# Kernel optimization log

Measured on AMD Instinct MI355X. Metric: run time of the kernel, lower is better.

## Reference

```python
import jax, jax.numpy as jnp
import numpy as np
from jax import lax

DIM = 256
HEADS = 8
C3 = DIM * 3 // 4  # 192
C1 = DIM // 4      # 64


def conv1x1(x, w):
    # x: [b,c,h,w], w: [o,c] (1x1 conv, no bias)
    return jnp.einsum('bchw,oc->bohw', x, w)


def dwconv3x3(x, w):
    # x: [b,c,h,w], w: [c,1,3,3] depthwise
    return lax.conv_general_dilated(
        x, w, window_strides=(1, 1), padding='SAME',
        feature_group_count=x.shape[1],
        dimension_numbers=('NCHW', 'OIHW', 'NCHW'))


def l2norm(x, eps=1e-12):
    # torch F.normalize: x / max(||x||, eps) along last dim
    n = jnp.sqrt(jnp.sum(x * x, axis=-1, keepdims=True))
    return x / jnp.maximum(n, eps)


def setup_inputs() -> dict:
    key = jax.random.key(0)
    ks = jax.random.split(key, 10)
    s = 0.02
    return {
        'x': jax.random.normal(ks[0], (4, DIM, 128, 128), jnp.float32),
        'k_v': jax.random.normal(ks[1], (4, 256), jnp.float32),
        'temperature': jnp.ones((HEADS, 1, 1), jnp.float32),
        'w_kR': jax.random.normal(ks[2], (C3, 192), jnp.float32) * s,
        'w_kI': jax.random.normal(ks[3], (C1, 64), jnp.float32) * s,
        'w_qR': jax.random.normal(ks[4], (DIM, C3), jnp.float32) * s,
        'w_qdw': jax.random.normal(ks[5], (DIM, 1, 3, 3), jnp.float32) * s,
        'w_kvI': jax.random.normal(ks[6], (2 * DIM, C1), jnp.float32) * s,
        'w_kvdw': jax.random.normal(ks[7], (2 * DIM, 1, 3, 3), jnp.float32) * s,
        'w_proj': jax.random.normal(ks[8], (DIM, DIM), jnp.float32) * s,
    }


def reference(x, k_v, temperature, w_kR, w_kI, w_qR, w_qdw, w_kvI, w_kvdw, w_proj):
    b, c, h, w = x.shape
    # FiLM-style modulation: x * kv + x
    kvr = (k_v[:, :192] @ w_kR.T)[:, :, None, None]  # [b, C3, 1, 1]
    kvi = (k_v[:, 192:] @ w_kI.T)[:, :, None, None]  # [b, C1, 1, 1]
    x_r = x[:, :C3] * kvr + x[:, :C3]
    x_i = x[:, C3:] * kvi + x[:, C3:]
    # QKV projections
    q = dwconv3x3(conv1x1(x_r, w_qR), w_qdw)          # [b, dim, h, w]
    kv = dwconv3x3(conv1x1(x_i, w_kvI), w_kvdw)       # [b, 2*dim, h, w]
    k, v = jnp.split(kv, 2, axis=1)
    hd = DIM // HEADS
    hw = h * w
    q = q.reshape(b, HEADS, hd, hw)
    k = k.reshape(b, HEADS, hd, hw)
    v = v.reshape(b, HEADS, hd, hw)
    # channel-wise (transposed) attention with L2 norm + temperature
    q = l2norm(q)
    k = l2norm(k)
    attn = jnp.einsum('bhcn,bhdn->bhcd', q, k) * temperature  # [b,H,hd,hd]
    attn = jax.nn.softmax(attn, axis=-1)
    out = jnp.einsum('bhcd,bhdn->bhcn', attn, v)
    out = out.reshape(b, DIM, h, w)
    return conv1x1(out, w_proj)
```

## Files before the change

### kernel.cpp

```cpp
#include <hip/hip_runtime.h>
#include <math.h>

#define HW 16384

typedef unsigned int uint;
typedef short bfrag __attribute__((ext_vector_type(8)));
typedef float f32x4 __attribute__((ext_vector_type(4)));

union FragCvt { uint4 u; bfrag v; };

__device__ inline uint pack2bf(float a, float b) {
  uint ua = __builtin_bit_cast(uint, a);
  uint ub = __builtin_bit_cast(uint, b);
  ua = (ua + 0x7FFFu + ((ua >> 16) & 1u)) >> 16;
  ub = (ub + 0x7FFFu + ((ub >> 16) & 1u)) & 0xFFFF0000u;
  return ua | ub;
}

__device__ inline void cvt_hilo(float4 a, float4 b, bfrag& hi, bfrag& lo) {
  float v0[8] = {a.x, a.y, a.z, a.w, b.x, b.y, b.z, b.w};
  uint hv[4], lv[4];
  #pragma unroll
  for (int i = 0; i < 4; ++i) {
    float x0 = v0[2 * i], x1 = v0[2 * i + 1];
    uint h = pack2bf(x0, x1);
    float h0 = __builtin_bit_cast(float, h << 16);
    float h1 = __builtin_bit_cast(float, h & 0xFFFF0000u);
    hv[i] = h;
    lv[i] = pack2bf(x0 - h0, x1 - h1);
  }
  FragCvt ch, cl;
  ch.u = make_uint4(hv[0], hv[1], hv[2], hv[3]);
  cl.u = make_uint4(lv[0], lv[1], lv[2], lv[3]);
  hi = ch.v;
  lo = cl.v;
}

#define LDS_BARRIER() do { \
  asm volatile("s_waitcnt lgkmcnt(0)" ::: "memory"); \
  __builtin_amdgcn_s_barrier(); \
} while (0)

__global__ __launch_bounds__(256) void mod_kernel(
    const float* __restrict__ kv, const float* __restrict__ wkR,
    const float* __restrict__ wkI, float* __restrict__ mod,
    float* __restrict__ S)
{
  int b = blockIdx.x;
  int c = threadIdx.x;
  float4 z4 = make_float4(0.f, 0.f, 0.f, 0.f);
  float4* sp = (float4*)(S + (((size_t)b * 256 + c) << 5));
  #pragma unroll
  for (int i = 0; i < 8; ++i) sp[i] = z4;

  const float* kvb = kv + b * 256;
  float s = 0.f;
  if (c < 192) {
    const float* wr = wkR + c * 192;
    for (int j = 0; j < 192; ++j) s += kvb[j] * wr[j];
  } else {
    const float* wi = wkI + (c - 192) * 64;
    for (int j = 0; j < 64; ++j) s += kvb[192 + j] * wi[j];
  }
  mod[b * 256 + c] = 1.f + s;
}

__device__ __forceinline__ void mgemm_body(
    const float* __restrict__ Wt, int ldW,
    const float* __restrict__ Xt,
    const float* __restrict__ modc,
    float* __restrict__ Yt,
    int K, int t, unsigned short* Al, unsigned short* Bl, float* Ml)
{
  int w = t >> 6, l = t & 63;
  int wm = (w >> 1) * 64, wn = (w & 1) * 64;
  int lm = l & 15, lk = (l >> 4) * 8;

  int am = t >> 1, ako = (t & 1) * 16;
  int bn = t & 127, bo = (t >> 7) * 8;

  Ml[t] = (modc && t < K) ? modc[t] : 1.f;

  f32x4 acc[4][4];
  #pragma unroll
  for (int fi = 0; fi < 4; ++fi)
    #pragma unroll
    for (int fj = 0; fj < 4; ++fj) acc[fi][fj] = {0.f, 0.f, 0.f, 0.f};

  float xrA[16], xrB[16];
  float4 wv0, wv1, wv2, wv3;

  auto load_x = [&](float* xr, int k0) {
    #pragma unroll
    for (int i = 0; i < 2; ++i) {
      int kb = k0 + bo + i * 16;
      #pragma unroll
      for (int r = 0; r < 8; ++r)
        xr[i * 8 + r] = Xt[(size_t)(kb + r) * HW + bn];
    }
  };
  auto load_w = [&](int k0) {
    const float* wsrc = Wt + (size_t)am * ldW + k0 + ako;
    wv0 = *(const float4*)(wsrc);
    wv1 = *(const float4*)(wsrc + 4);
    wv2 = *(const float4*)(wsrc + 8);
    wv3 = *(const float4*)(wsrc + 12);
  };
  auto pack_a = [&]() {
    uint4 aw0, aw1;
    aw0.x = pack2bf(wv0.x, wv0.y); aw0.y = pack2bf(wv0.z, wv0.w);
    aw0.z = pack2bf(wv1.x, wv1.y); aw0.w = pack2bf(wv1.z, wv1.w);
    aw1.x = pack2bf(wv2.x, wv2.y); aw1.y = pack2bf(wv2.z, wv2.w);
    aw1.z = pack2bf(wv3.x, wv3.y); aw1.w = pack2bf(wv3.z, wv3.w);
    *(uint4*)&Al[am * 40 + ako] = aw0;
    *(uint4*)&Al[am * 40 + ako + 8] = aw1;
  };
  auto pack_b = [&](const float* xr, int k0) {
    #pragma unroll
    for (int i = 0; i < 2; ++i) {
      float4 m0 = *(const float4*)&Ml[k0 + bo + i * 16];
      float4 m1 = *(const float4*)&Ml[k0 + bo + i * 16 + 4];
      uint4 bw;
      bw.x = pack2bf(xr[i * 8 + 0] * m0.x, xr[i * 8 + 1] * m0.y);
      bw.y = pack2bf(xr[i * 8 + 2] * m0.z, xr[i * 8 + 3] * m0.w);
      bw.z = pack2bf(xr[i * 8 + 4] * m1.x, xr[i * 8 + 5] * m1.y);
      bw.w = pack2bf(xr[i * 8 + 6] * m1.z, xr[i * 8 + 7] * m1.w);
      *(uint4*)&Bl[bn * 40 + bo + i * 16] = bw;
    }
  };
  auto mfma_step = [&]() {
    bfrag af[4], bfr[4];
    #pragma unroll
    for (int fj = 0; fj < 4; ++fj) {
      FragCvt cv;
      cv.u = *(const uint4*)&Al[(wm + fj * 16 + lm) * 40 + lk];
      af[fj] = cv.v;
    }
    #pragma unroll
    for (int fi = 0; fi < 4; ++fi) {
      FragCvt cv;
      cv.u = *(const uint4*)&Bl[(wn + fi * 16 + lm) * 40 + lk];
      bfr[fi] = cv.v;
    }
    #pragma unroll
    for (int fi = 0; fi < 4; ++fi)
      #pragma unroll
      for (int fj = 0; fj < 4; ++fj)
        acc[fi][fj] = __builtin_amdgcn_mfma_f32_16x16x32_bf16(
            bfr[fi], af[fj], acc[fi][fj], 0, 0, 0);
  };

  load_x(xrA, 0);
  load_x(xrB, 32);
  load_w(0);

  for (int k0 = 0; k0 < K; k0 += 64) {
    LDS_BARRIER();
    pack_a();
    if (k0 + 32 < K) load_w(k0 + 32);
    pack_b(xrA, k0);
    if (k0 + 64 < K) load_x(xrA, k0 + 64);
    LDS_BARRIER();
    mfma_step();

    LDS_BARRIER();
    pack_a();
    if (k0 + 64 < K) load_w(k0 + 64);
    pack_b(xrB, k0 + 32);
    if (k0 + 96 < K) load_x(xrB, k0 + 96);
    LDS_BARRIER();
    mfma_step();
  }

  int ph = (l >> 4) * 4;
  #pragma unroll
  for (int fi = 0; fi < 4; ++fi)
    #pragma unroll
    for (int fj = 0; fj < 4; ++fj)
      *(f32x4*)&Yt[(size_t)(wm + fj * 16 + lm) * HW + wn + fi * 16 + ph] =
          acc[fi][fj];
}

__global__ __launch_bounds__(256, 2) void mgemm_qk(
    const float* __restrict__ wqR, const float* __restrict__ wkvI,
    const float* __restrict__ X, const float* __restrict__ mod,
    float* __restrict__ Yq, float* __restrict__ Yk)
{
  __shared__ unsigned short Al[128 * 40];
  __shared__ unsigned short Bl[128 * 40];
  __shared__ float Ml[256];
  int b = blockIdx.z, mt = blockIdx.y, nt = blockIdx.x;
  if (mt < 2) {
    mgemm_body(wqR + (size_t)mt * 128 * 192, 192,
               X + (size_t)b * 4194304 + nt * 128,
               mod + b * 256,
               Yq + (size_t)b * 4194304 + (size_t)mt * 128 * HW + nt * 128,
               192, threadIdx.x, Al, Bl, Ml);
  } else {
    int m2 = mt - 2;
    mgemm_body(wkvI + (size_t)m2 * 128 * 64, 64,
               X + (size_t)b * 4194304 + (size_t)192 * HW + nt * 128,
               mod + b * 256 + 192,
               Yk + (size_t)b * 4194304 + (size_t)m2 * 128 * HW + nt * 128,
               64, threadIdx.x, Al, Bl, Ml);
  }
}

__global__ __launch_bounds__(256) void dwconv_kernel(
    const float* __restrict__ in, size_t in_bstride,
    const float* __restrict__ wdw,
    float* __restrict__ out, size_t out_bstride,
    float* __restrict__ ssq)
{
  int c = blockIdx.x;
  int b = blockIdx.y;
  int t = threadIdx.x;
  int r = t >> 5;
  int xq = t & 31;

  const float4* ip4 = (const float4*)(in + (size_t)b * in_bstride + ((size_t)c << 14));
  float4* op4 = (float4*)(out + (size_t)b * out_bstride + ((size_t)c << 14));
  const float* wp = wdw + c * 9;
  float w0 = wp[0], w1 = wp[1], w2 = wp[2], w3 = wp[3], w4 = wp[4],
        w5 = wp[5], w6 = wp[6], w7 = wp[7], w8 = wp[8];

  const float4 z4 = make_float4(0.f, 0.f, 0.f, 0.f);
  int y0 = r << 4;

  float4 a = (y0 > 0) ? ip4[((y0 - 1) << 5) + xq] : z4;
  float4 bb = ip4[(y0 << 5) + xq];

  float aL = __shfl_up(a.w, 1);  if (xq == 0)  aL = 0.f;
  float aR = __shfl_down(a.x, 1); if (xq == 31) aR = 0.f;
  float bL = __shfl_up(bb.w, 1); if (xq == 0)  bL = 0.f;
  float bR = __shfl_down(bb.x, 1); if (xq == 31) bR = 0.f;

  float ss = 0.f;
  #pragma unroll
  for (int i = 0; i < 16; ++i) {
    int y = y0 + i;
    int yc = (y + 1 < 128) ? (y + 1) : 127;
    float4 cc = ip4[(yc << 5) + xq];
    if (y + 1 >= 128) { cc.x = 0.f; cc.y = 0.f; cc.z = 0.f; cc.w = 0.f; }
    float cL = __shfl_up(cc.w, 1);  if (xq == 0)  cL = 0.f;
    float cR = __shfl_down(cc.x, 1); if (xq == 31) cR = 0.f;

    float4 o;
    o.x = w0 * aL  + w1 * a.x + w2 * a.y +
          w3 * bL  + w4 * bb.x + w5 * bb.y +
          w6 * cL  + w7 * cc.x + w8 * cc.y;
    o.y = w0 * a.x + w1 * a.y + w2 * a.z +
          w3 * bb.x + w4 * bb.y + w5 * bb.z +
          w6 * cc.x + w7 * cc.y + w8 * cc.z;
    o.z = w0 * a.y + w1 * a.z + w2 * a.w +
          w3 * bb.y + w4 * bb.z + w5 * bb.w +
          w6 * cc.y + w7 * cc.z + w8 * cc.w;
    o.w = w0 * a.z + w1 * a.w + w2 * aR +
          w3 * bb.z + w4 * bb.w + w5 * bR +
          w6 * cc.z + w7 * cc.w + w8 * cR;

    op4[(y << 5) + xq] = o;
    ss += o.x * o.x + o.y * o.y + o.z * o.z + o.w * o.w;

    a = bb; aL = bL; aR = bR;
    bb = cc; bL = cL; bR = cR;
  }

  if (ssq) {
    #pragma unroll
    for (int off = 32; off > 0; off >>= 1) ss += __shfl_down(ss, off);
    __shared__ float red[4];
    if ((t & 63) == 0) red[t >> 6] = ss;
    __syncthreads();
    if (t == 0) ssq[b * 256 + c] = red[0] + red[1] + red[2] + red[3];
  }
}

__global__ __launch_bounds__(256, 2) void gram_v_kernel(
    const float* __restrict__ qdw, const float* __restrict__ kdw,
    float* __restrict__ S,
    const float* __restrict__ wv, const float* __restrict__ X,
    const float* __restrict__ mod, float* __restrict__ Yv)
{
  __shared__ __align__(16) unsigned char smem[21504];
  int t = threadIdx.x;
  int b = blockIdx.z;

  if (blockIdx.x >= 16) {
    if (blockIdx.y >= 2) return;
    int nt = blockIdx.x - 16, mt = blockIdx.y;
    unsigned short* Al = (unsigned short*)smem;
    unsigned short* Bl = Al + 128 * 40;
    float* Ml = (float*)(smem + 20480);
    mgemm_body(wv + (size_t)mt * 128 * 64, 64,
               X + (size_t)b * 4194304 + (size_t)192 * HW + nt * 128,
               mod + b * 256 + 192,
               Yv + (size_t)b * 4194304 + (size_t)mt * 128 * HW + nt * 128,
               64, t, Al, Bl, Ml);
    return;
  }

  int chunk = blockIdx.x, h = blockIdx.y;
  int w = t >> 6, l = t & 63;
  int lm = l & 15;
  int lk8 = (l >> 4) * 8;

  const float* qh = qdw + (((size_t)b * 256 + h * 32) << 14);
  const float* kh = kdw + (((size_t)b * 256 + h * 32) << 14);
  const float* q0 = qh + ((size_t)lm << 14);
  const float* q1 = q0 + ((size_t)16 << 14);
  const float* k0 = kh + ((size_t)lm << 14);
  const float* k1 = k0 + ((size_t)16 << 14);

  int px0 = chunk * 1024 + w * 256 + lk8;

  f32x4 acc[2][2], accl[2][2];
  #pragma unroll
  for (int mi = 0; mi < 2; ++mi)
    #pragma unroll
    for (int nj = 0; nj < 2; ++nj) {
      acc[mi][nj] = {0.f, 0.f, 0.f, 0.f};
      accl[mi][nj] = {0.f, 0.f, 0.f, 0.f};
    }

  #pragma unroll 2
  for (int s = 0; s < 8; ++s) {
    int px = px0 + s * 32;
    float4 a0 = *(const float4*)(q0 + px);
    float4 a1 = *(const float4*)(q0 + px + 4);
    float4 a2 = *(const float4*)(q1 + px);
    float4 a3 = *(const float4*)(q1 + px + 4);
    float4 b0 = *(const float4*)(k0 + px);
    float4 b1 = *(const float4*)(k0 + px + 4);
    float4 b2 = *(const float4*)(k1 + px);
    float4 b3 = *(const float4*)(k1 + px + 4);

    bfrag qhF[2], qlF[2], khF[2], klF[2];
    cvt_hilo(a0, a1, qhF[0], qlF[0]);
    cvt_hilo(a2, a3, qhF[1], qlF[1]);
    cvt_hilo(b0, b1, khF[0], klF[0]);
    cvt_hilo(b2, b3, khF[1], klF[1]);

    #pragma unroll
    for (int mi = 0; mi < 2; ++mi)
      #pragma unroll
      for (int nj = 0; nj < 2; ++nj) {
        acc[mi][nj] = __builtin_amdgcn_mfma_f32_16x16x32_bf16(
            qhF[mi], khF[nj], acc[mi][nj], 0, 0, 0);
        accl[mi][nj] = __builtin_amdgcn_mfma_f32_16x16x32_bf16(
            qhF[mi], klF[nj], accl[mi][nj], 0, 0, 0);
        accl[mi][nj] = __builtin_amdgcn_mfma_f32_16x16x32_bf16(
            qlF[mi], khF[nj], accl[mi][nj], 0, 0, 0);
      }
  }

  float* red = (float*)smem;
  int orow = (l >> 4) * 4;
  #pragma unroll
  for (int mi = 0; mi < 2; ++mi)
    #pragma unroll
    for (int nj = 0; nj < 2; ++nj)
      #pragma unroll
      for (int r = 0; r < 4; ++r)
        red[w * 1024 + (mi * 16 + orow + r) * 32 + nj * 16 + lm] =
            acc[mi][nj][r] + accl[mi][nj][r];
  __syncthreads();
  float* Sp = S + (((size_t)b * 8 + h) << 10);
  for (int idx = t; idx < 1024; idx += 256)
    atomicAdd(&Sp[idx],
              red[idx] + red[1024 + idx] + red[2048 + idx] + red[3072 + idx]);
}

__global__ __launch_bounds__(256) void smb_vdw_kernel(
    const float* __restrict__ S, const float* __restrict__ ssq,
    const float* __restrict__ ssk, const float* __restrict__ temp,
    const float* __restrict__ wproj, float* __restrict__ M,
    const float* __restrict__ vpre, const float* __restrict__ wvdw,
    unsigned short* __restrict__ vdw)
{
  int t = threadIdx.x;
  int b = blockIdx.y;

  if (blockIdx.x >= 256) {
    int c = blockIdx.x - 256;
    int r = t >> 5;
    int xq = t & 31;
    const float4* ip4 =
        (const float4*)(vpre + (size_t)b * 4194304 + ((size_t)c << 14));
    uint2* op2 = (uint2*)(vdw + (size_t)b * 4194304 + ((size_t)c << 14));
    const float* wp = wvdw + c * 9;
    float w0 = wp[0], w1 = wp[1], w2 = wp[2], w3 = wp[3], w4 = wp[4],
          w5 = wp[5], w6 = wp[6], w7 = wp[7], w8 = wp[8];
    const float4 z4 = make_float4(0.f, 0.f, 0.f, 0.f);
    int y0 = r << 4;
    float4 a = (y0 > 0) ? ip4[((y0 - 1) << 5) + xq] : z4;
    float4 bb = ip4[(y0 << 5) + xq];
    float aL = __shfl_up(a.w, 1);  if (xq == 0)  aL = 0.f;
    float aR = __shfl_down(a.x, 1); if (xq == 31) aR = 0.f;
    float bL = __shfl_up(bb.w, 1); if (xq == 0)  bL = 0.f;
    float bR = __shfl_down(bb.x, 1); if (xq == 31) bR = 0.f;
    #pragma unroll
    for (int i = 0; i < 16; ++i) {
      int y = y0 + i;
      int yc = (y + 1 < 128) ? (y + 1) : 127;
      float4 cc = ip4[(yc << 5) + xq];
      if (y + 1 >= 128) { cc.x = 0.f; cc.y = 0.f; cc.z = 0.f; cc.w = 0.f; }
      float cL = __shfl_up(cc.w, 1);  if (xq == 0)  cL = 0.f;
      float cR = __shfl_down(cc.x, 1); if (xq == 31) cR = 0.f;
      float4 o;
      o.x = w0 * aL  + w1 * a.x + w2 * a.y +
            w3 * bL  + w4 * bb.x + w5 * bb.y +
            w6 * cL  + w7 * cc.x + w8 * cc.y;
      o.y = w0 * a.x + w1 * a.y + w2 * a.z +
            w3 * bb.x + w4 * bb.y + w5 * bb.z +
            w6 * cc.x + w7 * cc.y + w8 * cc.z;
      o.z = w0 * a.y + w1 * a.z + w2 * a.w +
            w3 * bb.y + w4 * bb.z + w5 * bb.w +
            w6 * cc.y + w7 * cc.z + w8 * cc.w;
      o.w = w0 * a.z + w1 * a.w + w2 * aR +
            w3 * bb.z + w4 * bb.w + w5 * bR +
            w6 * cc.z + w7 * cc.w + w8 * cR;
      uint2 ob;
      ob.x = pack2bf(o.x, o.y);
      ob.y = pack2bf(o.z, o.w);
      op2[(y << 5) + xq] = ob;
      a = bb; aL = bL; aR = bR;
      bb = cc; bL = cL; bR = cR;
    }
    return;
  }

  int o = blockIdx.x;
  __shared__ float At[8 * 32 * 33];
  __shared__ float Iq[256], Ik[256], Wp[256];

  Iq[t] = 1.f / fmaxf(sqrtf(ssq[b * 256 + t]), 1e-12f);
  Ik[t] = 1.f / fmaxf(sqrtf(ssk[b * 256 + t]), 1e-12f);
  Wp[t] = wproj[o * 256 + t];
  __syncthreads();

  int h = t >> 5, c = t & 31;
  const float* row = S + (((size_t)b * 8 + h) << 10) + c * 32;
  float invq = Iq[h * 32 + c];
  float T = temp[h];
  float lg[32];
  float mx = -1e30f;
  #pragma unroll
  for (int d = 0; d < 32; ++d) {
    float v = row[d] * invq * Ik[h * 32 + d] * T;
    lg[d] = v;
    mx = fmaxf(mx, v);
  }
  float sum = 0.f;
  #pragma unroll
  for (int d = 0; d < 32; ++d) { float e = expf(lg[d] - mx); lg[d] = e; sum += e; }
  float inv = 1.f / sum;
  float* arow = &At[(h * 32 + c) * 33];
  #pragma unroll
  for (int d = 0; d < 32; ++d) arow[d] = lg[d] * inv;
  __syncthreads();

  int d2 = t & 31, h2 = t >> 5;
  float s = 0.f;
  #pragma unroll
  for (int cc = 0; cc < 32; ++cc)
    s += Wp[h2 * 32 + cc] * At[(h2 * 32 + cc) * 33 + d2];
  M[((size_t)b * 256 + o) * 256 + t] = s;
}

__global__ __launch_bounds__(256, 2) void mgemm_bx(
    const float* __restrict__ Mw, const unsigned short* __restrict__ Xb,
    float* __restrict__ out)
{
  __shared__ unsigned short Al[128 * 40];
  __shared__ unsigned short Bl[128 * 40];
  int b = blockIdx.z, mt = blockIdx.y, nt = blockIdx.x;
  const float* Wt = Mw + (size_t)b * 65536 + (size_t)mt * 128 * 256;
  const unsigned short* Xt = Xb + (size_t)b * 4194304 + nt * 128;
  float* Yt = out + (size_t)b * 4194304 + (size_t)mt * 128 * HW + nt * 128;
  int t = threadIdx.x;
  const int K = 256;

  int w = t >> 6, l = t & 63;
  int wm = (w >> 1) * 64, wn = (w & 1) * 64;
  int lm = l & 15, lk = (l >> 4) * 8;
  int am = t >> 1, ako = (t & 1) * 16;
  int bn = t & 127, bo = (t >> 7) * 8;

  f32x4 acc[4][4];
  #pragma unroll
  for (int fi = 0; fi < 4; ++fi)
    #pragma unroll
    for (int fj = 0; fj < 4; ++fj) acc[fi][fj] = {0.f, 0.f, 0.f, 0.f};

  unsigned short xrA[16], xrB[16];
  float4 wv0, wv1, wv2, wv3;

  auto load_x = [&](unsigned short* xr, int k0) {
    #pragma unroll
    for (int i = 0; i < 2; ++i) {
      int kb = k0 + bo + i * 16;
      #pragma unroll
      for (int r = 0; r < 8; ++r)
        xr[i * 8 + r] = Xt[(size_t)(kb + r) * HW + bn];
    }
  };
  auto load_w = [&](int k0) {
    const float* wsrc = Wt + (size_t)am * 256 + k0 + ako;
    wv0 = *(const float4*)(wsrc);
    wv1 = *(const float4*)(wsrc + 4);
    wv2 = *(const float4*)(wsrc + 8);
    wv3 = *(const float4*)(wsrc + 12);
  };
  auto pack_a = [&]() {
    uint4 aw0, aw1;
    aw0.x = pack2bf(wv0.x, wv0.y); aw0.y = pack2bf(wv0.z, wv0.w);
    aw0.z = pack2bf(wv1.x, wv1.y); aw0.w = pack2bf(wv1.z, wv1.w);
    aw1.x = pack2bf(wv2.x, wv2.y); aw1.y = pack2bf(wv2.z, wv2.w);
    aw1.z = pack2bf(wv3.x, wv3.y); aw1.w = pack2bf(wv3.z, wv3.w);
    *(uint4*)&Al[am * 40 + ako] = aw0;
    *(uint4*)&Al[am * 40 + ako + 8] = aw1;
  };
  auto pack_b = [&](const unsigned short* xr) {
    #pragma unroll
    for (int i = 0; i < 2; ++i) {
      uint4 bw;
      bw.x = (uint)xr[i * 8 + 0] | ((uint)xr[i * 8 + 1] << 16);
      bw.y = (uint)xr[i * 8 + 2] | ((uint)xr[i * 8 + 3] << 16);
      bw.z = (uint)xr[i * 8 + 4] | ((uint)xr[i * 8 + 5] << 16);
      bw.w = (uint)xr[i * 8 + 6] | ((uint)xr[i * 8 + 7] << 16);
      *(uint4*)&Bl[bn * 40 + bo + i * 16] = bw;
    }
  };
  auto mfma_step = [&]() {
    bfrag af[4], bfr[4];
    #pragma unroll
    for (int fj = 0; fj < 4; ++fj) {
      FragCvt cv;
      cv.u = *(const uint4*)&Al[(wm + fj * 16 + lm) * 40 + lk];
      af[fj] = cv.v;
    }
    #pragma unroll
    for (int fi = 0; fi < 4; ++fi) {
      FragCvt cv;
      cv.u = *(const uint4*)&Bl[(wn + fi * 16 + lm) * 40 + lk];
      bfr[fi] = cv.v;
    }
    #pragma unroll
    for (int fi = 0; fi < 4; ++fi)
      #pragma unroll
      for (int fj = 0; fj < 4; ++fj)
        acc[fi][fj] = __builtin_amdgcn_mfma_f32_16x16x32_bf16(
            bfr[fi], af[fj], acc[fi][fj], 0, 0, 0);
  };

  load_x(xrA, 0);
  load_x(xrB, 32);
  load_w(0);

  for (int k0 = 0; k0 < K; k0 += 64) {
    LDS_BARRIER();
    pack_a();
    if (k0 + 32 < K) load_w(k0 + 32);
    pack_b(xrA);
    if (k0 + 64 < K) load_x(xrA, k0 + 64);
    LDS_BARRIER();
    mfma_step();

    LDS_BARRIER();
    pack_a();
    if (k0 + 64 < K) load_w(k0 + 64);
    pack_b(xrB);
    if (k0 + 96 < K) load_x(xrB, k0 + 96);
    LDS_BARRIER();
    mfma_step();
  }

  int ph = (l >> 4) * 4;
  #pragma unroll
  for (int fi = 0; fi < 4; ++fi)
    #pragma unroll
    for (int fj = 0; fj < 4; ++fj)
      *(f32x4*)&Yt[(size_t)(wm + fj * 16 + lm) * HW + wn + fi * 16 + ph] =
          acc[fi][fj];
}

extern "C" void kernel_launch(void* const* d_in, const int* in_sizes, int n_in,
                              void* d_out, int out_size, void* d_ws, size_t ws_size,
                              hipStream_t stream)
{
  const float* x      = (const float*)d_in[0];
  const float* k_v    = (const float*)d_in[1];
  const float* temp   = (const float*)d_in[2];
  const float* w_kR   = (const float*)d_in[3];
  const float* w_kI   = (const float*)d_in[4];
  const float* w_qR   = (const float*)d_in[5];
  const float* w_qdw  = (const float*)d_in[6];
  const float* w_kvI  = (const float*)d_in[7];
  const float* w_kvdw = (const float*)d_in[8];
  const float* w_proj = (const float*)d_in[9];
  float* out = (float*)d_out;

  float* ws   = (float*)d_ws;
  float* bufA = ws;
  float* bufB = ws + 16777216;
  float* bufC = ws + 33554432;
  float* sm   = ws + 50331648;
  float* mod  = sm;
  float* ssq  = sm + 1024;
  float* ssk  = sm + 2048;
  float* S    = sm + 3072;
  float* M    = sm + 3072 + 32768;

  mod_kernel<<<dim3(4), dim3(256), 0, stream>>>(k_v, w_kR, w_kI, mod, S);

  mgemm_qk<<<dim3(128, 4, 4), dim3(256), 0, stream>>>(
      w_qR, w_kvI, x, mod, bufA, bufB);

  dwconv_kernel<<<dim3(256, 4), dim3(256), 0, stream>>>(
      bufB, 4194304, w_kvdw, bufC, 4194304, ssk);

  dwconv_kernel<<<dim3(256, 4), dim3(256), 0, stream>>>(
      bufA, 4194304, w_qdw, bufB, 4194304, ssq);

  gram_v_kernel<<<dim3(144, 8, 4), dim3(256), 0, stream>>>(
      bufB, bufC, S, w_kvI + 256 * 64, x, mod, bufA);

  smb_vdw_kernel<<<dim3(512, 4), dim3(256), 0, stream>>>(
      S, ssq, ssk, temp, w_proj, M,
      bufA, w_kvdw + 256 * 9, (unsigned short*)bufC);

  mgemm_bx<<<dim3(128, 2, 4), dim3(256), 0, stream>>>(
      M, (const unsigned short*)bufC, out);
}
```

Measured before the change: 304.2 us.

## Fuse V projection into QK GEMM and merge depthwise convs in place

The V 1x1 projection moves into the first GEMM launch as two extra M-tiles. The three depthwise convolutions (q, k, v) are merged into one in-place kernel; it keeps outputs in registers and writes them back after a barrier, and for v it writes bf16 into the fp32 buffer's footprint. The Gram and score kernels lose their piggybacked V work, and the final GEMM reads v with a doubled channel stride. This cuts launches and the separate v pass. In exchange the Gram kernel no longer overlaps with V work, and the in-place dwconv has higher register pressure.

After: 302.5 us. Within noise of the previous version (-0.5%).

```diff
diff --git a/kernel.cpp b/kernel.cpp
--- a/kernel.cpp
+++ b/kernel.cpp
@@ -181,10 +181,10 @@
           acc[fi][fj];
 }
 
-__global__ __launch_bounds__(256, 2) void mgemm_qk(
+__global__ __launch_bounds__(256, 2) void mgemm_qkv(
     const float* __restrict__ wqR, const float* __restrict__ wkvI,
     const float* __restrict__ X, const float* __restrict__ mod,
-    float* __restrict__ Yq, float* __restrict__ Yk)
+    float* __restrict__ Yq, float* __restrict__ Yk, float* __restrict__ Yv)
 {
   __shared__ unsigned short Al[128 * 40];
   __shared__ unsigned short Bl[128 * 40];
@@ -196,31 +196,44 @@
                mod + b * 256,
                Yq + (size_t)b * 4194304 + (size_t)mt * 128 * HW + nt * 128,
                192, threadIdx.x, Al, Bl, Ml);
-  } else {
+  } else if (mt < 4) {
     int m2 = mt - 2;
     mgemm_body(wkvI + (size_t)m2 * 128 * 64, 64,
                X + (size_t)b * 4194304 + (size_t)192 * HW + nt * 128,
                mod + b * 256 + 192,
                Yk + (size_t)b * 4194304 + (size_t)m2 * 128 * HW + nt * 128,
                64, threadIdx.x, Al, Bl, Ml);
-  }
-}
-
-__global__ __launch_bounds__(256) void dwconv_kernel(
-    const float* __restrict__ in, size_t in_bstride,
-    const float* __restrict__ wdw,
-    float* __restrict__ out, size_t out_bstride,
-    float* __restrict__ ssq)
-{
-  int c = blockIdx.x;
+  } else {
+    int m2 = mt - 4;
+    mgemm_body(wkvI + (size_t)(256 + m2 * 128) * 64, 64,
+               X + (size_t)b * 4194304 + (size_t)192 * HW + nt * 128,
+               mod + b * 256 + 192,
+               Yv + (size_t)b * 4194304 + (size_t)m2 * 128 * HW + nt * 128,
+               64, threadIdx.x, Al, Bl, Ml);
+  }
+}
+
+__global__ __launch_bounds__(256) void dw3_kernel(
+    float* __restrict__ qbuf, float* __restrict__ kbuf, float* __restrict__ vbuf,
+    const float* __restrict__ wqdw, const float* __restrict__ wkvdw,
+    float* __restrict__ ssq, float* __restrict__ ssk)
+{
+  int g = blockIdx.x;
   int b = blockIdx.y;
+  int c = g & 255;
+  int which = g >> 8;
+
+  float* buf = (which == 0) ? kbuf : ((which == 1) ? qbuf : vbuf);
+  const float* wp = (which == 1) ? (wqdw + c * 9)
+                  : (which == 0) ? (wkvdw + c * 9)
+                                 : (wkvdw + (256 + c) * 9);
+
   int t = threadIdx.x;
   int r = t >> 5;
   int xq = t & 31;
 
-  const float4* ip4 = (const float4*)(in + (size_t)b * in_bstride + ((size_t)c << 14));
-  float4* op4 = (float4*)(out + (size_t)b * out_bstride + ((size_t)c << 14));
-  const float* wp = wdw + c * 9;
+  float* plane = buf + (size_t)b * 4194304 + ((size_t)c << 14);
+  const float4* ip4 = (const float4*)plane;
   float w0 = wp[0], w1 = wp[1], w2 = wp[2], w3 = wp[3], w4 = wp[4],
         w5 = wp[5], w6 = wp[6], w7 = wp[7], w8 = wp[8];
 
@@ -236,6 +249,7 @@
   float bR = __shfl_down(bb.x, 1); if (xq == 31) bR = 0.f;
 
   float ss = 0.f;
+  float4 ores[16];
   #pragma unroll
   for (int i = 0; i < 16; ++i) {
     int y = y0 + i;
@@ -259,48 +273,47 @@
           w3 * bb.z + w4 * bb.w + w5 * bR +
           w6 * cc.z + w7 * cc.w + w8 * cR;
 
-    op4[(y << 5) + xq] = o;
+    ores[i] = o;
     ss += o.x * o.x + o.y * o.y + o.z * o.z + o.w * o.w;
 
     a = bb; aL = bL; aR = bR;
     bb = cc; bL = cL; bR = cR;
   }
 
-  if (ssq) {
+  __syncthreads();
+
+  if (which < 2) {
+    float4* op4 = (float4*)plane;
+    #pragma unroll
+    for (int i = 0; i < 16; ++i) op4[((y0 + i) << 5) + xq] = ores[i];
+  } else {
+    uint2* op2 = (uint2*)plane;
+    #pragma unroll
+    for (int i = 0; i < 16; ++i) {
+      uint2 ob;
+      ob.x = pack2bf(ores[i].x, ores[i].y);
+      ob.y = pack2bf(ores[i].z, ores[i].w);
+      op2[((y0 + i) << 5) + xq] = ob;
+    }
+  }
+
+  if (which < 2) {
+    float* ssp = (which == 0) ? ssk : ssq;
     #pragma unroll
     for (int off = 32; off > 0; off >>= 1) ss += __shfl_down(ss, off);
     __shared__ float red[4];
     if ((t & 63) == 0) red[t >> 6] = ss;
     __syncthreads();
-    if (t == 0) ssq[b * 256 + c] = red[0] + red[1] + red[2] + red[3];
-  }
-}
-
-__global__ __launch_bounds__(256, 2) void gram_v_kernel(
+    if (t == 0) ssp[b * 256 + c] = red[0] + red[1] + red[2] + red[3];
+  }
+}
+
+__global__ __launch_bounds__(256) void gram_kernel(
     const float* __restrict__ qdw, const float* __restrict__ kdw,
-    float* __restrict__ S,
-    const float* __restrict__ wv, const float* __restrict__ X,
-    const float* __restrict__ mod, float* __restrict__ Yv)
-{
-  __shared__ __align__(16) unsigned char smem[21504];
+    float* __restrict__ S)
+{
+  int chunk = blockIdx.x, h = blockIdx.y, b = blockIdx.z;
   int t = threadIdx.x;
-  int b = blockIdx.z;
-
-  if (blockIdx.x >= 16) {
-    if (blockIdx.y >= 2) return;
-    int nt = blockIdx.x - 16, mt = blockIdx.y;
-    unsigned short* Al = (unsigned short*)smem;
-    unsigned short* Bl = Al + 128 * 40;
-    float* Ml = (float*)(smem + 20480);
-    mgemm_body(wv + (size_t)mt * 128 * 64, 64,
-               X + (size_t)b * 4194304 + (size_t)192 * HW + nt * 128,
-               mod + b * 256 + 192,
-               Yv + (size_t)b * 4194304 + (size_t)mt * 128 * HW + nt * 128,
-               64, t, Al, Bl, Ml);
-    return;
-  }
-
-  int chunk = blockIdx.x, h = blockIdx.y;
   int w = t >> 6, l = t & 63;
   int lm = l & 15;
   int lk8 = (l >> 4) * 8;
@@ -354,7 +367,7 @@
       }
   }
 
-  float* red = (float*)smem;
+  __shared__ float red[4][1024];
   int orow = (l >> 4) * 4;
   #pragma unroll
   for (int mi = 0; mi < 2; ++mi)
@@ -362,75 +375,21 @@
     for (int nj = 0; nj < 2; ++nj)
       #pragma unroll
       for (int r = 0; r < 4; ++r)
-        red[w * 1024 + (mi * 16 + orow + r) * 32 + nj * 16 + lm] =
+        red[w][(mi * 16 + orow + r) * 32 + nj * 16 + lm] =
             acc[mi][nj][r] + accl[mi][nj][r];
   __syncthreads();
   float* Sp = S + (((size_t)b * 8 + h) << 10);
   for (int idx = t; idx < 1024; idx += 256)
-    atomicAdd(&Sp[idx],
-              red[idx] + red[1024 + idx] + red[2048 + idx] + red[3072 + idx]);
-}
-
-__global__ __launch_bounds__(256) void smb_vdw_kernel(
+    atomicAdd(&Sp[idx], red[0][idx] + red[1][idx] + red[2][idx] + red[3][idx]);
+}
+
+__global__ __launch_bounds__(256) void smb_kernel(
     const float* __restrict__ S, const float* __restrict__ ssq,
     const float* __restrict__ ssk, const float* __restrict__ temp,
-    const float* __restrict__ wproj, float* __restrict__ M,
-    const float* __restrict__ vpre, const float* __restrict__ wvdw,
-    unsigned short* __restrict__ vdw)
-{
+    const float* __restrict__ wproj, float* __restrict__ M)
+{
+  int o = blockIdx.x, b = blockIdx.y;
   int t = threadIdx.x;
-  int b = blockIdx.y;
-
-  if (blockIdx.x >= 256) {
-    int c = blockIdx.x - 256;
-    int r = t >> 5;
-    int xq = t & 31;
-    const float4* ip4 =
-        (const float4*)(vpre + (size_t)b * 4194304 + ((size_t)c << 14));
-    uint2* op2 = (uint2*)(vdw + (size_t)b * 4194304 + ((size_t)c << 14));
-    const float* wp = wvdw + c * 9;
-    float w0 = wp[0], w1 = wp[1], w2 = wp[2], w3 = wp[3], w4 = wp[4],
-          w5 = wp[5], w6 = wp[6], w7 = wp[7], w8 = wp[8];
-    const float4 z4 = make_float4(0.f, 0.f, 0.f, 0.f);
-    int y0 = r << 4;
-    float4 a = (y0 > 0) ? ip4[((y0 - 1) << 5) + xq] : z4;
-    float4 bb = ip4[(y0 << 5) + xq];
-    float aL = __shfl_up(a.w, 1);  if (xq == 0)  aL = 0.f;
-    float aR = __shfl_down(a.x, 1); if (xq == 31) aR = 0.f;
-    float bL = __shfl_up(bb.w, 1); if (xq == 0)  bL = 0.f;
-    float bR = __shfl_down(bb.x, 1); if (xq == 31) bR = 0.f;
-    #pragma unroll
-    for (int i = 0; i < 16; ++i) {
-      int y = y0 + i;
-      int yc = (y + 1 < 128) ? (y + 1) : 127;
-      float4 cc = ip4[(yc << 5) + xq];
-      if (y + 1 >= 128) { cc.x = 0.f; cc.y = 0.f; cc.z = 0.f; cc.w = 0.f; }
-      float cL = __shfl_up(cc.w, 1);  if (xq == 0)  cL = 0.f;
-      float cR = __shfl_down(cc.x, 1); if (xq == 31) cR = 0.f;
-      float4 o;
-      o.x = w0 * aL  + w1 * a.x + w2 * a.y +
-            w3 * bL  + w4 * bb.x + w5 * bb.y +
-            w6 * cL  + w7 * cc.x + w8 * cc.y;
-      o.y = w0 * a.x + w1 * a.y + w2 * a.z +
-            w3 * bb.x + w4 * bb.y + w5 * bb.z +
-            w6 * cc.x + w7 * cc.y + w8 * cc.z;
-      o.z = w0 * a.y + w1 * a.z + w2 * a.w +
-            w3 * bb.y + w4 * bb.z + w5 * bb.w +
-            w6 * cc.y + w7 * cc.z + w8 * cc.w;
-      o.w = w0 * a.z + w1 * a.w + w2 * aR +
-            w3 * bb.z + w4 * bb.w + w5 * bR +
-            w6 * cc.z + w7 * cc.w + w8 * cR;
-      uint2 ob;
-      ob.x = pack2bf(o.x, o.y);
-      ob.y = pack2bf(o.z, o.w);
-      op2[(y << 5) + xq] = ob;
-      a = bb; aL = bL; aR = bR;
-      bb = cc; bL = cL; bR = cR;
-    }
-    return;
-  }
-
-  int o = blockIdx.x;
   __shared__ float At[8 * 32 * 33];
   __shared__ float Iq[256], Ik[256], Wp[256];
 
@@ -476,7 +435,7 @@
   __shared__ unsigned short Bl[128 * 40];
   int b = blockIdx.z, mt = blockIdx.y, nt = blockIdx.x;
   const float* Wt = Mw + (size_t)b * 65536 + (size_t)mt * 128 * 256;
-  const unsigned short* Xt = Xb + (size_t)b * 4194304 + nt * 128;
+  const unsigned short* Xt = Xb + (size_t)b * 8388608 + nt * 128;
   float* Yt = out + (size_t)b * 4194304 + (size_t)mt * 128 * HW + nt * 128;
   int t = threadIdx.x;
   const int K = 256;
@@ -502,7 +461,7 @@
       int kb = k0 + bo + i * 16;
       #pragma unroll
       for (int r = 0; r < 8; ++r)
-        xr[i * 8 + r] = Xt[(size_t)(kb + r) * HW + bn];
+        xr[i * 8 + r] = Xt[(size_t)(kb + r) * 32768 + bn];
     }
   };
   auto load_w = [&](int k0) {
@@ -614,21 +573,16 @@
 
   mod_kernel<<<dim3(4), dim3(256), 0, stream>>>(k_v, w_kR, w_kI, mod, S);
 
-  mgemm_qk<<<dim3(128, 4, 4), dim3(256), 0, stream>>>(
-      w_qR, w_kvI, x, mod, bufA, bufB);
-
-  dwconv_kernel<<<dim3(256, 4), dim3(256), 0, stream>>>(
-      bufB, 4194304, w_kvdw, bufC, 4194304, ssk);
-
-  dwconv_kernel<<<dim3(256, 4), dim3(256), 0, stream>>>(
-      bufA, 4194304, w_qdw, bufB, 4194304, ssq);
-
-  gram_v_kernel<<<dim3(144, 8, 4), dim3(256), 0, stream>>>(
-      bufB, bufC, S, w_kvI + 256 * 64, x, mod, bufA);
-
-  smb_vdw_kernel<<<dim3(512, 4), dim3(256), 0, stream>>>(
-      S, ssq, ssk, temp, w_proj, M,
-      bufA, w_kvdw + 256 * 9, (unsigned short*)bufC);
+  mgemm_qkv<<<dim3(128, 6, 4), dim3(256), 0, stream>>>(
+      w_qR, w_kvI, x, mod, bufA, bufB, bufC);
+
+  dw3_kernel<<<dim3(768, 4), dim3(256), 0, stream>>>(
+      bufA, bufB, bufC, w_qdw, w_kvdw, ssq, ssk);
+
+  gram_kernel<<<dim3(16, 8, 4), dim3(256), 0, stream>>>(bufA, bufB, S);
+
+  smb_kernel<<<dim3(256, 4), dim3(256), 0, stream>>>(
+      S, ssq, ssk, temp, w_proj, M);
 
   mgemm_bx<<<dim3(128, 2, 4), dim3(256), 0, stream>>>(
       M, (const unsigned short*)bufC, out);
```
